# Kernel optimization log

Hardware: AMD Instinct MI355X
Metric: run time of the kernel (lower is better)

## Reference

```python
import jax, jax.numpy as jnp
import numpy as np

N = 50000    # nodes
E = 800000   # edges (avg degree 16)
IN, H, OUT = 128, 16, 300


def setup_inputs() -> dict:
    key = jax.random.key(0)
    ks = jax.random.split(key, 8)
    x = jax.random.normal(ks[0], (N, IN), jnp.float32)
    edge_index = jax.random.randint(ks[1], (2, E), 0, N, jnp.int32)

    def w(k, i, o):
        return jax.random.normal(k, (i, o), jnp.float32) / np.float32(np.sqrt(i))

    return dict(
        x=x, edge_index=edge_index,
        W1=w(ks[2], IN, H), b1=jnp.zeros((H,), jnp.float32),
        Wl1=w(ks[3], IN, H), bl1=jnp.zeros((H,), jnp.float32),
        W2=w(ks[4], H, H), b2=jnp.zeros((H,), jnp.float32),
        Wl2=w(ks[5], H, H), bl2=jnp.zeros((H,), jnp.float32),
        Wo=w(ks[6], H, OUT), bo=jnp.zeros((OUT,), jnp.float32),
    )


def gcn_conv(x, W, b, src, dst, n):
    """PyG GCNConv: x@W, symmetric norm with self-loops, scatter-add, + bias."""
    h = x @ W                                    # [N, F_out]
    ones = jnp.ones(src.shape[0], h.dtype)
    deg = jax.ops.segment_sum(ones, dst, num_segments=n) + 1.0  # +1 self-loop
    dinv = jax.lax.rsqrt(deg)                    # deg >= 1, safe
    norm = dinv[src] * dinv[dst]                 # [E]
    agg = jax.ops.segment_sum(h[src] * norm[:, None], dst, num_segments=n)
    agg = agg + h * (dinv * dinv)[:, None]       # self-loop message
    return agg + b


def reference(x, edge_index, W1, b1, Wl1, bl1, W2, b2, Wl2, bl2, Wo, bo):
    src, dst = edge_index[0], edge_index[1]
    n = x.shape[0]
    # layer 1: conv.relu + skip linear  (dropout p=0 / inference -> identity)
    h = jax.nn.relu(gcn_conv(x, W1, b1, src, dst, n)) + (x @ Wl1 + bl1)
    # layer 2
    h = jax.nn.relu(gcn_conv(h, W2, b2, src, dst, n)) + (h @ Wl2 + bl2)
    # output conv + log_softmax over classes
    out = gcn_conv(h, Wo, bo, src, dst, n)
    return jax.nn.log_softmax(out, axis=1)
```

## Files before the change

kernel.cpp:

```cpp
#include <hip/hip_runtime.h>
#include <hip/hip_bf16.h>

#define NN   50000
#define EE   800000
#define INF_ 128
#define HH   16
#define OUTC 300

#define NB   196
#define CAP  4608
#define CHK  4096
#define GB_  196

#define W1_OFF   0
#define WL1_OFF  2048
#define B1_OFF   4096
#define BL1_OFF  4112
#define W2_OFF   4128
#define WL2_OFF  4384
#define B2_OFF   4640
#define BL2_OFF  4656
#define WO_OFF   4672
#define BO_OFF   9472
#define WC_TOT   9772

__device__ __forceinline__ float bfu2f(unsigned short u) {
    return __uint_as_float(((unsigned)u) << 16);
}
__device__ __forceinline__ unsigned short f2bfu(float f) {
    __hip_bfloat16 h = __float2bfloat16(f);
    return *reinterpret_cast<unsigned short*>(&h);
}
__device__ __forceinline__ unsigned packbf(float lo, float hi) {
    return (unsigned)f2bfu(lo) | ((unsigned)f2bfu(hi) << 16);
}
__device__ __forceinline__ float cvt1(const void* p, int i, int flag) {
    return flag ? ((const float*)p)[i] : bfu2f(((const unsigned short*)p)[i]);
}

__global__ __launch_bounds__(64) void detect_kernel(const unsigned* __restrict__ xw, int* __restrict__ flag) {
    int t = threadIdx.x;
    int hits = 0;
#pragma unroll
    for (int q = 0; q < 4; q++) {
        unsigned w = xw[t * 4 + q];
        float lo = __uint_as_float(w << 16);
        if (!(fabsf(lo) < 1e4f)) hits++;
    }
#pragma unroll
    for (int o = 32; o > 0; o >>= 1) hits += __shfl_xor(hits, o);
    if (t == 0) flag[0] = (hits > 8) ? 1 : 0;
}

__global__ __launch_bounds__(256) void convert_kernel(
    const void* __restrict__ W1, const void* __restrict__ Wl1,
    const void* __restrict__ b1, const void* __restrict__ bl1,
    const void* __restrict__ W2, const void* __restrict__ Wl2,
    const void* __restrict__ b2, const void* __restrict__ bl2,
    const void* __restrict__ Wo, const void* __restrict__ bo,
    const int* __restrict__ flagp, float* __restrict__ wc)
{
    int t = blockIdx.x * 256 + threadIdx.x;
    if (t >= WC_TOT) return;
    const int flag = flagp[0];
    float v;
    if      (t < WL1_OFF) v = cvt1(W1,  t - W1_OFF,  flag);
    else if (t < B1_OFF)  v = cvt1(Wl1, t - WL1_OFF, flag);
    else if (t < BL1_OFF) v = cvt1(b1,  t - B1_OFF,  flag);
    else if (t < W2_OFF)  v = cvt1(bl1, t - BL1_OFF, flag);
    else if (t < WL2_OFF) v = cvt1(W2,  t - W2_OFF,  flag);
    else if (t < B2_OFF)  v = cvt1(Wl2, t - WL2_OFF, flag);
    else if (t < BL2_OFF) v = cvt1(b2,  t - B2_OFF,  flag);
    else if (t < WO_OFF)  v = cvt1(bl2, t - BL2_OFF, flag);
    else if (t < BO_OFF)  v = cvt1(Wo,  t - WO_OFF,  flag);
    else                  v = cvt1(bo,  t - BO_OFF,  flag);
    wc[t] = v;
}

__global__ __launch_bounds__(256) void bplace_kernel(
    const int* __restrict__ src, const int* __restrict__ dst,
    int* __restrict__ gcur, uint2* __restrict__ gpairs)
{
    __shared__ uint2 raw[CHK];
    __shared__ uint2 srt[CHK];
    __shared__ unsigned char bid[CHK];
    __shared__ int cnt[NB];
    __shared__ int loff[NB];
    __shared__ int cur2[NB];
    __shared__ int gbase[NB];
    __shared__ int sc[256];

    int tid = threadIdx.x;
    int e0 = blockIdx.x * CHK;
    int n = min(CHK, EE - e0);
    if (n <= 0) return;
    for (int t = tid; t < NB; t += 256) cnt[t] = 0;
    __syncthreads();

    for (int j = tid; j < n; j += 256) {
        unsigned s = (unsigned)src[e0 + j];
        unsigned d = (unsigned)dst[e0 + j];
        raw[j] = make_uint2(s, d);
        atomicAdd(&cnt[d >> 8], 1);
    }
    __syncthreads();

    int v = (tid < NB) ? cnt[tid] : 0;
    sc[tid] = v;
    __syncthreads();
    for (int d = 1; d < 256; d <<= 1) {
        int u = (tid >= d) ? sc[tid - d] : 0;
        __syncthreads();
        sc[tid] += u;
        __syncthreads();
    }
    if (tid < NB) { loff[tid] = sc[tid] - v; cur2[tid] = sc[tid] - v; }
    __syncthreads();

    for (int j = tid; j < n; j += 256) {
        uint2 p = raw[j];
        int b = (int)(p.y >> 8);
        int pos = atomicAdd(&cur2[b], 1);
        srt[pos] = p;
        bid[pos] = (unsigned char)b;
    }
    __syncthreads();

    if (tid < NB) {
        int c = cnt[tid];
        gbase[tid] = c ? atomicAdd(&gcur[tid], c) : 0;
    }
    __syncthreads();

    for (int j = tid; j < n; j += 256) {
        int b = bid[j];
        int p = gbase[b] + (j - loff[b]);
        if (p < CAP) gpairs[(size_t)b * CAP + p] = srt[j];
    }
}

__global__ __launch_bounds__(256) void bscan_kernel(
    const int* __restrict__ gcur, int* __restrict__ gboff, int* __restrict__ off)
{
    __shared__ int sc[256];
    int t = threadIdx.x;
    int v = (t < NB) ? gcur[t] : 0;
    sc[t] = v;
    __syncthreads();
    for (int d = 1; d < 256; d <<= 1) {
        int u = (t >= d) ? sc[t - d] : 0;
        __syncthreads();
        sc[t] += u;
        __syncthreads();
    }
    if (t < NB) gboff[t] = sc[t] - v;
    if (t == 0) { gboff[NB] = EE; off[NN] = EE; }
}

__global__ __launch_bounds__(256) void cplace_kernel(
    const uint2* __restrict__ gpairs, const int* __restrict__ gcur,
    const int* __restrict__ gboff, int* __restrict__ off,
    float* __restrict__ dinv, int* __restrict__ csr_src)
{
    __shared__ uint2 pl[CAP];
    __shared__ int ncnt[256];
    __shared__ int nscan[256];
    __shared__ int noff[256];
    __shared__ int ncur[256];
    int b = blockIdx.x, t = threadIdx.x;
    int c = min(gcur[b], CAP);
    int gb = gboff[b];
    int nb = b << 8;

    ncnt[t] = 0;
    for (int j = t; j < c; j += 256) pl[j] = gpairs[(size_t)b * CAP + j];
    __syncthreads();

    for (int j = t; j < c; j += 256) atomicAdd(&ncnt[pl[j].y & 255], 1);
    __syncthreads();

    int v = ncnt[t];
    nscan[t] = v;
    __syncthreads();
    for (int d = 1; d < 256; d <<= 1) {
        int u = (t >= d) ? nscan[t - d] : 0;
        __syncthreads();
        nscan[t] += u;
        __syncthreads();
    }
    int excl = nscan[t] - v;
    noff[t] = excl;
    ncur[t] = excl;

    int node = nb + t;
    if (node < NN) {
        off[node] = gb + excl;
        dinv[node] = rsqrtf((float)v + 1.0f);
    }
    __syncthreads();

    for (int j = t; j < c; j += 256) {
        uint2 p = pl[j];
        int d = (int)(p.y & 255);
        int pos = atomicAdd(&ncur[d], 1);
        csr_src[gb + pos] = (int)p.x;
    }
}

__global__ __launch_bounds__(256) void lin1_kernel(
    const void* __restrict__ xp, const float* __restrict__ wc,
    const float* __restrict__ dinv, const int* __restrict__ flagp,
    unsigned short* __restrict__ A, unsigned short* __restrict__ B)
{
    __shared__ float2 sWL[INF_ * HH];
    __shared__ float sb[HH];
    for (int t = threadIdx.x; t < INF_ * HH; t += 256)
        sWL[t] = make_float2(wc[W1_OFF + t], wc[WL1_OFF + t]);
    if (threadIdx.x < HH) sb[threadIdx.x] = wc[BL1_OFF + threadIdx.x];
    __syncthreads();

    int i = blockIdx.x * 256 + threadIdx.x;
    if (i >= NN) return;
    const int flag = flagp[0];

    float a[HH], l[HH];
#pragma unroll
    for (int f = 0; f < HH; f++) { a[f] = 0.f; l[f] = 0.f; }

    for (int k0 = 0; k0 < INF_ / 8; k0++) {
        float xv[8];
        if (flag) {
            const float4* xr = (const float4*)((const float*)xp + (size_t)i * INF_);
            float4 r0 = xr[k0 * 2], r1 = xr[k0 * 2 + 1];
            xv[0] = r0.x; xv[1] = r0.y; xv[2] = r0.z; xv[3] = r0.w;
            xv[4] = r1.x; xv[5] = r1.y; xv[6] = r1.z; xv[7] = r1.w;
        } else {
            const uint4* xr = (const uint4*)((const unsigned short*)xp + (size_t)i * INF_);
            uint4 v = xr[k0];
            unsigned uu[4] = { v.x, v.y, v.z, v.w };
#pragma unroll
            for (int q = 0; q < 4; q++) {
                xv[q * 2]     = __uint_as_float(uu[q] << 16);
                xv[q * 2 + 1] = __uint_as_float(uu[q] & 0xffff0000u);
            }
        }
#pragma unroll
        for (int j = 0; j < 8; j++) {
            float xj = xv[j];
            int k = k0 * 8 + j;
#pragma unroll
            for (int f = 0; f < HH; f++) {
                float2 wv = sWL[k * HH + f];
                a[f] = fmaf(xj, wv.x, a[f]);
                l[f] = fmaf(xj, wv.y, l[f]);
            }
        }
    }
    float di = dinv[i];
    unsigned pa[8], pb[8];
#pragma unroll
    for (int h = 0; h < 8; h++) {
        pa[h] = packbf(a[2 * h] * di, a[2 * h + 1] * di);
        pb[h] = packbf(l[2 * h] + sb[2 * h], l[2 * h + 1] + sb[2 * h + 1]);
    }
    uint4* Ar = (uint4*)(A + (size_t)i * HH);
    uint4* Br = (uint4*)(B + (size_t)i * HH);
    Ar[0] = make_uint4(pa[0], pa[1], pa[2], pa[3]);
    Ar[1] = make_uint4(pa[4], pa[5], pa[6], pa[7]);
    Br[0] = make_uint4(pb[0], pb[1], pb[2], pb[3]);
    Br[1] = make_uint4(pb[4], pb[5], pb[6], pb[7]);
}

__global__ __launch_bounds__(256) void gather_combine_kernel(
    const int* __restrict__ off, const int* __restrict__ csr,
    const float* __restrict__ dinv, const unsigned short* __restrict__ X,
    unsigned short* __restrict__ Y, const float* __restrict__ bias, int mode)
{
    int wid = (blockIdx.x * 256 + threadIdx.x) >> 6;
    int lane = threadIdx.x & 63;
    if (wid >= NN) return;
    int e = lane >> 2, q = lane & 3;
    int s0 = off[wid], s1 = off[wid + 1];
    float a0 = 0.f, a1 = 0.f, a2 = 0.f, a3 = 0.f;
    for (int base = s0; base < s1; base += 16) {
        int p = base + e;
        bool valid = (p < s1);
        int s = valid ? csr[p] : 0;
        uint2 v = ((const uint2*)X)[(size_t)s * 4 + q];
        if (valid) {
            a0 += __uint_as_float(v.x << 16);
            a1 += __uint_as_float(v.x & 0xffff0000u);
            a2 += __uint_as_float(v.y << 16);
            a3 += __uint_as_float(v.y & 0xffff0000u);
        }
    }
#pragma unroll
    for (int m = 4; m <= 32; m <<= 1) {
        a0 += __shfl_xor(a0, m);
        a1 += __shfl_xor(a1, m);
        a2 += __shfl_xor(a2, m);
        a3 += __shfl_xor(a3, m);
    }
    if (lane < 4) {
        float di = dinv[wid];
        uint2 xv = ((const uint2*)X)[(size_t)wid * 4 + lane];
        float x0 = __uint_as_float(xv.x << 16);
        float x1 = __uint_as_float(xv.x & 0xffff0000u);
        float x2 = __uint_as_float(xv.y << 16);
        float x3 = __uint_as_float(xv.y & 0xffff0000u);
        float o0, o1, o2, o3;
        if (mode == 2) {
            o0 = di * (a0 + x0); o1 = di * (a1 + x1);
            o2 = di * (a2 + x2); o3 = di * (a3 + x3);
        } else {
            uint2 yv = ((const uint2*)Y)[(size_t)wid * 4 + lane];
            float y0 = __uint_as_float(yv.x << 16);
            float y1 = __uint_as_float(yv.x & 0xffff0000u);
            float y2 = __uint_as_float(yv.y << 16);
            float y3 = __uint_as_float(yv.y & 0xffff0000u);
            o0 = fmaxf(di * (a0 + x0) + bias[lane * 4 + 0], 0.f) + y0;
            o1 = fmaxf(di * (a1 + x1) + bias[lane * 4 + 1], 0.f) + y1;
            o2 = fmaxf(di * (a2 + x2) + bias[lane * 4 + 2], 0.f) + y2;
            o3 = fmaxf(di * (a3 + x3) + bias[lane * 4 + 3], 0.f) + y3;
            if (mode) { o0 *= di; o1 *= di; o2 *= di; o3 *= di; }
        }
        ((uint2*)Y)[(size_t)wid * 4 + lane] = make_uint2(packbf(o0, o1), packbf(o2, o3));
    }
}

__global__ __launch_bounds__(256) void lin2_kernel(
    unsigned short* __restrict__ B, const float* __restrict__ wc,
    const float* __restrict__ dinv, unsigned short* __restrict__ A)
{
    __shared__ float2 sWL[HH * HH];
    __shared__ float sb[HH];
    for (int t = threadIdx.x; t < HH * HH; t += 256)
        sWL[t] = make_float2(wc[W2_OFF + t], wc[WL2_OFF + t]);
    if (threadIdx.x < HH) sb[threadIdx.x] = wc[BL2_OFF + threadIdx.x];
    __syncthreads();

    int i = blockIdx.x * 256 + threadIdx.x;
    if (i >= NN) return;

    float z[HH];
    const uint4* br = (const uint4*)(B + (size_t)i * HH);
    uint4 r0 = br[0], r1 = br[1];
    unsigned uu[8] = { r0.x, r0.y, r0.z, r0.w, r1.x, r1.y, r1.z, r1.w };
#pragma unroll
    for (int h = 0; h < 8; h++) {
        z[2 * h]     = __uint_as_float(uu[h] << 16);
        z[2 * h + 1] = __uint_as_float(uu[h] & 0xffff0000u);
    }
    float a[HH], l[HH];
#pragma unroll
    for (int f = 0; f < HH; f++) { a[f] = 0.f; l[f] = 0.f; }
#pragma unroll
    for (int k = 0; k < HH; k++) {
        float zk = z[k];
#pragma unroll
        for (int f = 0; f < HH; f++) {
            float2 wv = sWL[k * HH + f];
            a[f] = fmaf(zk, wv.x, a[f]);
            l[f] = fmaf(zk, wv.y, l[f]);
        }
    }
    float di = dinv[i];
    unsigned pa[8], pb[8];
#pragma unroll
    for (int h = 0; h < 8; h++) {
        pa[h] = packbf(a[2 * h] * di, a[2 * h + 1] * di);
        pb[h] = packbf(l[2 * h] + sb[2 * h], l[2 * h + 1] + sb[2 * h + 1]);
    }
    uint4* Ar = (uint4*)(A + (size_t)i * HH);
    uint4* Br = (uint4*)(B + (size_t)i * HH);
    Ar[0] = make_uint4(pa[0], pa[1], pa[2], pa[3]);
    Ar[1] = make_uint4(pa[4], pa[5], pa[6], pa[7]);
    Br[0] = make_uint4(pb[0], pb[1], pb[2], pb[3]);
    Br[1] = make_uint4(pb[4], pb[5], pb[6], pb[7]);
}

__global__ __launch_bounds__(256) void final_kernel(
    const unsigned short* __restrict__ Z, const float* __restrict__ wc,
    const int* __restrict__ flagp, void* __restrict__ outp)
{
    __shared__ float sW[HH * OUTC];
    __shared__ float sbb[OUTC];
    for (int t = threadIdx.x; t < HH * OUTC; t += 256) sW[t] = wc[WO_OFF + t];
    for (int t = threadIdx.x; t < OUTC; t += 256)      sbb[t] = wc[BO_OFF + t];
    __syncthreads();

    const int flag = flagp[0];
    int wave = threadIdx.x >> 6, lane = threadIdx.x & 63;
    int i0 = blockIdx.x * 16 + wave * 4;

    float zf[4];
#pragma unroll
    for (int n = 0; n < 4; n++) zf[n] = bfu2f(Z[(size_t)(i0 + n) * HH + (lane & 15)]);

    float y[4][5];
#pragma unroll
    for (int jj = 0; jj < 5; jj++) {
        int j = lane + jj * 64;
        float b = (j < OUTC) ? sbb[j] : 0.f;
#pragma unroll
        for (int n = 0; n < 4; n++) y[n][jj] = b;
    }

#pragma unroll
    for (int k = 0; k < HH; k++) {
        float zb[4];
#pragma unroll
        for (int n = 0; n < 4; n++) zb[n] = __shfl(zf[n], k);
#pragma unroll
        for (int jj = 0; jj < 5; jj++) {
            int j = lane + jj * 64;
            float w = (j < OUTC) ? sW[k * OUTC + j] : 0.f;
#pragma unroll
            for (int n = 0; n < 4; n++) y[n][jj] = fmaf(zb[n], w, y[n][jj]);
        }
    }

#pragma unroll
    for (int n = 0; n < 4; n++) {
        float m = -1e30f;
#pragma unroll
        for (int jj = 0; jj < 5; jj++) {
            int j = lane + jj * 64;
            if (j < OUTC) m = fmaxf(m, y[n][jj]);
        }
#pragma unroll
        for (int o = 32; o > 0; o >>= 1) m = fmaxf(m, __shfl_xor(m, o));
        float s = 0.f;
#pragma unroll
        for (int jj = 0; jj < 5; jj++) {
            int j = lane + jj * 64;
            if (j < OUTC) s += __expf(y[n][jj] - m);
        }
#pragma unroll
        for (int o = 32; o > 0; o >>= 1) s += __shfl_xor(s, o);
        float lse = m + __logf(s);
#pragma unroll
        for (int jj = 0; jj < 5; jj++) {
            int j = lane + jj * 64;
            if (j < OUTC) {
                float v = y[n][jj] - lse;
                size_t ofs = (size_t)(i0 + n) * OUTC + j;
                if (flag) ((float*)outp)[ofs] = v;
                else      ((__hip_bfloat16*)outp)[ofs] = __float2bfloat16(v);
            }
        }
    }
}

extern "C" void kernel_launch(void* const* d_in, const int* in_sizes, int n_in,
                              void* d_out, int out_size, void* d_ws, size_t ws_size,
                              hipStream_t stream) {
    const void* x   = d_in[0];
    const int*  ei  = (const int*)d_in[1];
    const void* W1  = d_in[2];
    const void* b1  = d_in[3];
    const void* Wl1 = d_in[4];
    const void* bl1 = d_in[5];
    const void* W2  = d_in[6];
    const void* b2  = d_in[7];
    const void* Wl2 = d_in[8];
    const void* bl2 = d_in[9];
    const void* Wo  = d_in[10];
    const void* bo  = d_in[11];

    const int* srcp = ei;
    const int* dstp = ei + EE;

    char* wsb = (char*)d_ws;
    int*   flag    = (int*)wsb;
    float* wc      = (float*)(wsb + 4 * 16);
    int*   gcur    = (int*)(wsb + 4 * 10000);
    int*   gboff   = (int*)(wsb + 4 * 10200);
    int*   off     = (int*)(wsb + 4 * 10400);
    int*   csr_src = (int*)(wsb + 4 * 60416);
    float* dinv    = (float*)(wsb + 4 * 860416);
    uint2* gpairs  = (uint2*)(wsb + 4 * 910416);
    unsigned short* A = (unsigned short*)(wsb + 4 * 2716752);
    unsigned short* B = (unsigned short*)(wsb + 4 * 3116752);

    const int gN = (NN + 255) / 256;
    const int gG = (NN * 64 + 255) / 256;
    const int gW = (WC_TOT + 255) / 256;

    detect_kernel<<<1, 64, 0, stream>>>((const unsigned*)x, flag);
    convert_kernel<<<gW, 256, 0, stream>>>(W1, Wl1, b1, bl1, W2, Wl2, b2, bl2,
                                           Wo, bo, flag, wc);

    hipMemsetAsync(gcur, 0, NB * sizeof(int), stream);
    bplace_kernel<<<GB_, 256, 0, stream>>>(srcp, dstp, gcur, gpairs);
    bscan_kernel<<<1, 256, 0, stream>>>(gcur, gboff, off);
    cplace_kernel<<<NB, 256, 0, stream>>>(gpairs, gcur, gboff, off, dinv, csr_src);

    lin1_kernel<<<gN, 256, 0, stream>>>(x, wc, dinv, flag, A, B);
    gather_combine_kernel<<<gG, 256, 0, stream>>>(off, csr_src, dinv, A, B, wc + B1_OFF, 0);

    lin2_kernel<<<gN, 256, 0, stream>>>(B, wc, dinv, A);
    gather_combine_kernel<<<gG, 256, 0, stream>>>(off, csr_src, dinv, A, B, wc + B2_OFF, 1);

    gather_combine_kernel<<<gG, 256, 0, stream>>>(off, csr_src, dinv, B, A, wc + B2_OFF, 2);

    final_kernel<<<(NN + 15) / 16, 256, 0, stream>>>(A, wc, flag, d_out);
}
```

Measured before the change: 251.4 us.

## Pack four nodes per wavefront in gather and fuse small setup kernels

The gather/combine kernel now gives each wavefront 4 destination nodes with 16 lanes each, instead of one node per wavefront. Each group loads up to 16 CSR indices at once, broadcasts them by shuffle and gathers 4 edges per round, so the shuffle reduction is shorter and far fewer wavefronts are launched. Separately, the datatype-detect pass and the gcur memset are folded into convert_kernel, and the bucket scan is recomputed inside each cplace block, removing three small launches. The cost is redundant per-block work (every block redoes the flag detection and the 196-entry scan) and some idle lanes in the gather when the 4 nodes have uneven degrees.

```diff
diff --git a/kernel.cpp b/kernel.cpp
--- a/kernel.cpp
+++ b/kernel.cpp
@@ -38,31 +38,32 @@
     return flag ? ((const float*)p)[i] : bfu2f(((const unsigned short*)p)[i]);
 }
 
-__global__ __launch_bounds__(64) void detect_kernel(const unsigned* __restrict__ xw, int* __restrict__ flag) {
-    int t = threadIdx.x;
-    int hits = 0;
-#pragma unroll
-    for (int q = 0; q < 4; q++) {
-        unsigned w = xw[t * 4 + q];
-        float lo = __uint_as_float(w << 16);
-        if (!(fabsf(lo) < 1e4f)) hits++;
-    }
-#pragma unroll
-    for (int o = 32; o > 0; o >>= 1) hits += __shfl_xor(hits, o);
-    if (t == 0) flag[0] = (hits > 8) ? 1 : 0;
-}
-
 __global__ __launch_bounds__(256) void convert_kernel(
     const void* __restrict__ W1, const void* __restrict__ Wl1,
     const void* __restrict__ b1, const void* __restrict__ bl1,
     const void* __restrict__ W2, const void* __restrict__ Wl2,
     const void* __restrict__ b2, const void* __restrict__ bl2,
     const void* __restrict__ Wo, const void* __restrict__ bo,
-    const int* __restrict__ flagp, float* __restrict__ wc)
-{
-    int t = blockIdx.x * 256 + threadIdx.x;
+    const unsigned* __restrict__ xw, int* __restrict__ flagp,
+    int* __restrict__ gcur, float* __restrict__ wc)
+{
+    __shared__ int shits;
+    int tid = threadIdx.x;
+    if (tid == 0) shits = 0;
+    __syncthreads();
+    unsigned w = xw[tid];
+    float lo = __uint_as_float(w << 16);
+    if (!(fabsf(lo) < 1e4f)) atomicAdd(&shits, 1);
+    __syncthreads();
+    const int flag = (shits > 8) ? 1 : 0;
+
+    if (blockIdx.x == 0) {
+        if (tid == 0) flagp[0] = flag;
+        if (tid < NB) gcur[tid] = 0;
+    }
+
+    int t = blockIdx.x * 256 + tid;
     if (t >= WC_TOT) return;
-    const int flag = flagp[0];
     float v;
     if      (t < WL1_OFF) v = cvt1(W1,  t - W1_OFF,  flag);
     else if (t < B1_OFF)  v = cvt1(Wl1, t - WL1_OFF, flag);
@@ -139,13 +140,19 @@
     }
 }
 
-__global__ __launch_bounds__(256) void bscan_kernel(
-    const int* __restrict__ gcur, int* __restrict__ gboff, int* __restrict__ off)
-{
+__global__ __launch_bounds__(256) void cplace_kernel(
+    const uint2* __restrict__ gpairs, const int* __restrict__ gcur,
+    int* __restrict__ off, float* __restrict__ dinv, int* __restrict__ csr_src)
+{
+    __shared__ uint2 pl[CAP];
     __shared__ int sc[256];
-    int t = threadIdx.x;
-    int v = (t < NB) ? gcur[t] : 0;
-    sc[t] = v;
+    __shared__ int ncnt[256];
+    __shared__ int nscan[256];
+    __shared__ int ncur[256];
+    int b = blockIdx.x, t = threadIdx.x;
+
+    int bv = (t < NB) ? gcur[t] : 0;
+    sc[t] = bv;
     __syncthreads();
     for (int d = 1; d < 256; d <<= 1) {
         int u = (t >= d) ? sc[t - d] : 0;
@@ -153,26 +160,15 @@
         sc[t] += u;
         __syncthreads();
     }
-    if (t < NB) gboff[t] = sc[t] - v;
-    if (t == 0) { gboff[NB] = EE; off[NN] = EE; }
-}
-
-__global__ __launch_bounds__(256) void cplace_kernel(
-    const uint2* __restrict__ gpairs, const int* __restrict__ gcur,
-    const int* __restrict__ gboff, int* __restrict__ off,
-    float* __restrict__ dinv, int* __restrict__ csr_src)
-{
-    __shared__ uint2 pl[CAP];
-    __shared__ int ncnt[256];
-    __shared__ int nscan[256];
-    __shared__ int noff[256];
-    __shared__ int ncur[256];
-    int b = blockIdx.x, t = threadIdx.x;
+    __shared__ int gb_s;
+    if (t == b) gb_s = sc[t] - bv;
+    if (b == 0 && t == 0) off[NN] = EE;
+    ncnt[t] = 0;
+    __syncthreads();
+    int gb = gb_s;
+
     int c = min(gcur[b], CAP);
-    int gb = gboff[b];
     int nb = b << 8;
-
-    ncnt[t] = 0;
     for (int j = t; j < c; j += 256) pl[j] = gpairs[(size_t)b * CAP + j];
     __syncthreads();
 
@@ -189,7 +185,6 @@
         __syncthreads();
     }
     int excl = nscan[t] - v;
-    noff[t] = excl;
     ncur[t] = excl;
 
     int node = nb + t;
@@ -276,34 +271,48 @@
     const float* __restrict__ dinv, const unsigned short* __restrict__ X,
     unsigned short* __restrict__ Y, const float* __restrict__ bias, int mode)
 {
-    int wid = (blockIdx.x * 256 + threadIdx.x) >> 6;
     int lane = threadIdx.x & 63;
-    if (wid >= NN) return;
-    int e = lane >> 2, q = lane & 3;
-    int s0 = off[wid], s1 = off[wid + 1];
+    int w = (blockIdx.x * 256 + threadIdx.x) >> 6;
+    int n = lane >> 4, j = lane & 15;
+    int node = w * 4 + n;
+    int s0 = off[node], s1 = off[node + 1];
+    int deg = s1 - s0;
+
+    int wmax = deg;
+    wmax = max(wmax, __shfl_xor(wmax, 16));
+    wmax = max(wmax, __shfl_xor(wmax, 32));
+
+    const uint2* X4 = (const uint2*)X;
     float a0 = 0.f, a1 = 0.f, a2 = 0.f, a3 = 0.f;
-    for (int base = s0; base < s1; base += 16) {
-        int p = base + e;
-        bool valid = (p < s1);
-        int s = valid ? csr[p] : 0;
-        uint2 v = ((const uint2*)X)[(size_t)s * 4 + q];
-        if (valid) {
-            a0 += __uint_as_float(v.x << 16);
-            a1 += __uint_as_float(v.x & 0xffff0000u);
-            a2 += __uint_as_float(v.y << 16);
-            a3 += __uint_as_float(v.y & 0xffff0000u);
-        }
-    }
-#pragma unroll
-    for (int m = 4; m <= 32; m <<= 1) {
+    int eh = j >> 2, q = j & 3;
+
+    for (int base = 0; base < wmax; base += 16) {
+        int p = s0 + base + j;
+        int sj = (p < s1) ? csr[p] : 0;
+#pragma unroll
+        for (int r = 0; r < 4; r++) {
+            int e = r * 4 + eh;
+            int se = __shfl(sj, (n << 4) + e);
+            bool val = (base + e) < deg;
+            uint2 v = X4[(size_t)(val ? se : node) * 4 + q];
+            if (val) {
+                a0 += __uint_as_float(v.x << 16);
+                a1 += __uint_as_float(v.x & 0xffff0000u);
+                a2 += __uint_as_float(v.y << 16);
+                a3 += __uint_as_float(v.y & 0xffff0000u);
+            }
+        }
+    }
+#pragma unroll
+    for (int m = 4; m <= 8; m <<= 1) {
         a0 += __shfl_xor(a0, m);
         a1 += __shfl_xor(a1, m);
         a2 += __shfl_xor(a2, m);
         a3 += __shfl_xor(a3, m);
     }
-    if (lane < 4) {
-        float di = dinv[wid];
-        uint2 xv = ((const uint2*)X)[(size_t)wid * 4 + lane];
+    if (eh == 0) {
+        float di = dinv[node];
+        uint2 xv = X4[(size_t)node * 4 + q];
         float x0 = __uint_as_float(xv.x << 16);
         float x1 = __uint_as_float(xv.x & 0xffff0000u);
         float x2 = __uint_as_float(xv.y << 16);
@@ -313,18 +322,18 @@
             o0 = di * (a0 + x0); o1 = di * (a1 + x1);
             o2 = di * (a2 + x2); o3 = di * (a3 + x3);
         } else {
-            uint2 yv = ((const uint2*)Y)[(size_t)wid * 4 + lane];
+            uint2 yv = ((const uint2*)Y)[(size_t)node * 4 + q];
             float y0 = __uint_as_float(yv.x << 16);
             float y1 = __uint_as_float(yv.x & 0xffff0000u);
             float y2 = __uint_as_float(yv.y << 16);
             float y3 = __uint_as_float(yv.y & 0xffff0000u);
-            o0 = fmaxf(di * (a0 + x0) + bias[lane * 4 + 0], 0.f) + y0;
-            o1 = fmaxf(di * (a1 + x1) + bias[lane * 4 + 1], 0.f) + y1;
-            o2 = fmaxf(di * (a2 + x2) + bias[lane * 4 + 2], 0.f) + y2;
-            o3 = fmaxf(di * (a3 + x3) + bias[lane * 4 + 3], 0.f) + y3;
+            o0 = fmaxf(di * (a0 + x0) + bias[q * 4 + 0], 0.f) + y0;
+            o1 = fmaxf(di * (a1 + x1) + bias[q * 4 + 1], 0.f) + y1;
+            o2 = fmaxf(di * (a2 + x2) + bias[q * 4 + 2], 0.f) + y2;
+            o3 = fmaxf(di * (a3 + x3) + bias[q * 4 + 3], 0.f) + y3;
             if (mode) { o0 *= di; o1 *= di; o2 *= di; o3 *= di; }
         }
-        ((uint2*)Y)[(size_t)wid * 4 + lane] = make_uint2(packbf(o0, o1), packbf(o2, o3));
+        ((uint2*)Y)[(size_t)node * 4 + q] = make_uint2(packbf(o0, o1), packbf(o2, o3));
     }
 }
 
@@ -475,7 +484,6 @@
     int*   flag    = (int*)wsb;
     float* wc      = (float*)(wsb + 4 * 16);
     int*   gcur    = (int*)(wsb + 4 * 10000);
-    int*   gboff   = (int*)(wsb + 4 * 10200);
     int*   off     = (int*)(wsb + 4 * 10400);
     int*   csr_src = (int*)(wsb + 4 * 60416);
     float* dinv    = (float*)(wsb + 4 * 860416);
@@ -483,26 +491,23 @@
     unsigned short* A = (unsigned short*)(wsb + 4 * 2716752);
     unsigned short* B = (unsigned short*)(wsb + 4 * 3116752);
 
-    const int gN = (NN + 255) / 256;
-    const int gG = (NN * 64 + 255) / 256;
-    const int gW = (WC_TOT + 255) / 256;
-
-    detect_kernel<<<1, 64, 0, stream>>>((const unsigned*)x, flag);
+    const int gN  = (NN + 255) / 256;
+    const int gG4 = (NN / 4 * 64) / 256;
+    const int gW  = (WC_TOT + 255) / 256;
+
     convert_kernel<<<gW, 256, 0, stream>>>(W1, Wl1, b1, bl1, W2, Wl2, b2, bl2,
-                                           Wo, bo, flag, wc);
-
-    hipMemsetAsync(gcur, 0, NB * sizeof(int), stream);
+                                           Wo, bo, (const unsigned*)x, flag, gcur, wc);
+
     bplace_kernel<<<GB_, 256, 0, stream>>>(srcp, dstp, gcur, gpairs);
-    bscan_kernel<<<1, 256, 0, stream>>>(gcur, gboff, off);
-    cplace_kernel<<<NB, 256, 0, stream>>>(gpairs, gcur, gboff, off, dinv, csr_src);
+    cplace_kernel<<<NB, 256, 0, stream>>>(gpairs, gcur, off, dinv, csr_src);
 
     lin1_kernel<<<gN, 256, 0, stream>>>(x, wc, dinv, flag, A, B);
-    gather_combine_kernel<<<gG, 256, 0, stream>>>(off, csr_src, dinv, A, B, wc + B1_OFF, 0);
+    gather_combine_kernel<<<gG4, 256, 0, stream>>>(off, csr_src, dinv, A, B, wc + B1_OFF, 0);
 
     lin2_kernel<<<gN, 256, 0, stream>>>(B, wc, dinv, A);
-    gather_combine_kernel<<<gG, 256, 0, stream>>>(off, csr_src, dinv, A, B, wc + B2_OFF, 1);
-
-    gather_combine_kernel<<<gG, 256, 0, stream>>>(off, csr_src, dinv, B, A, wc + B2_OFF, 2);
-
-    final_kernel<<<(NN + 15) / 16, 256, 0, stream>>>(A, wc, flag, d_out);
-}
+    gather_combine_kernel<<<gG4, 256, 0, stream>>>(off, csr_src, dinv, A, B, wc + B2_OFF, 1);
+
+    gather_combine_kernel<<<gG4, 256, 0, stream>>>(off, csr_src, dinv, B, A, wc + B2_OFF, 2);
+
+    final_kernel<<<gG4, 256, 0, stream>>>(A, wc, flag, d_out);
+}
```

After: 225.2 us. 1.12x faster.
